# Kernel tuning notes

Measured on AMD Instinct MI355X. Metric: run time of the kernel, lower is better.

Reference implementation:

```python
import jax, jax.numpy as jnp
import numpy as np

EMB = 1024
HEADS = 16
EPS = 1e-6


def setup_inputs() -> dict:
    key = jax.random.key(0)
    ks = jax.random.split(key, 12)
    B, S, D = 2, 2048, EMB
    scale = 1.0 / np.sqrt(D)
    inp = {
        "v": jax.random.normal(ks[0], (B, S, D), jnp.float32),
        "k": jax.random.normal(ks[1], (B, S, D), jnp.float32),
        "q": jax.random.normal(ks[2], (B, S, D), jnp.float32),
        "Wv": jax.random.normal(ks[3], (D, D), jnp.float32) * scale,
        "bv": jnp.zeros((D,), jnp.float32),
        "Wk": jax.random.normal(ks[4], (D, D), jnp.float32) * scale,
        "bk": jnp.zeros((D,), jnp.float32),
        "Wq": jax.random.normal(ks[5], (D, D), jnp.float32) * scale,
        "bq": jnp.zeros((D,), jnp.float32),
        "Wo": jax.random.normal(ks[6], (D, D), jnp.float32) * scale,
        "bo": jnp.zeros((D,), jnp.float32),
        "gamma": jnp.ones((D,), jnp.float32),
        "beta": jnp.zeros((D,), jnp.float32),
    }
    return inp


def reference(v, k, q, Wv, bv, Wk, bk, Wq, bq, Wo, bo, gamma, beta):
    B, S, D = q.shape
    H = HEADS
    d = D // H  # head depth

    def split_heads(x):  # [B,S,D] -> [B,H,S,d]
        return x.reshape(B, S, H, d).transpose(0, 2, 1, 3)

    V = split_heads(v @ Wv + bv)
    K = split_heads(k @ Wk + bk)
    Q = split_heads(q @ Wq + bq)

    # scaled dot-product attention (full score matrix, no mask)
    scores = jnp.einsum("bhqd,bhkd->bhqk", Q, K) / jnp.sqrt(jnp.float32(d))
    attn = jax.nn.softmax(scores, axis=-1)
    ctx = jnp.einsum("bhqk,bhkd->bhqd", attn, V)

    ctx = ctx.transpose(0, 2, 1, 3).reshape(B, S, D)
    out = ctx @ Wo + bo + q  # final dense + residual

    # LayerNormalization(epsilon=1e-6) over last axis
    mu = jnp.mean(out, axis=-1, keepdims=True)
    var = jnp.var(out, axis=-1, keepdims=True)
    return gamma * (out - mu) * jax.lax.rsqrt(var + EPS) + beta
```

## Files before the change

kernel.cpp:

```cpp
#include <hip/hip_runtime.h>
#include <hip/hip_bf16.h>
#include <math.h>

#define D_EMB 1024
#define NBATCH 2
#define SEQ 2048
#define NH 16
#define HDIM 64
#define MTOT (NBATCH*SEQ)
#define NT (SEQ/64)

typedef unsigned short u16;
typedef __attribute__((ext_vector_type(8))) short bf16x8;
typedef __attribute__((ext_vector_type(4))) float f32x4;
typedef __attribute__((ext_vector_type(16))) float f32x16;
typedef __attribute__((ext_vector_type(4))) unsigned short u16x4;
typedef __attribute__((ext_vector_type(4))) unsigned int u32x4;

__device__ __forceinline__ u16 f2b(float f) {
  union { float f; unsigned u; } x; x.f = f;
  unsigned r = x.u + 0x7fffu + ((x.u >> 16) & 1u);
  return (u16)(r >> 16);
}

__device__ __forceinline__ void gld_lds16(const u16* g, u16* l) {
  __builtin_amdgcn_global_load_lds(
      (const __attribute__((address_space(1))) void*)g,
      (__attribute__((address_space(3))) void*)l, 16, 0, 0);
}

__global__ __launch_bounds__(256) void convert_qkv(
    const float* __restrict__ v, const float* __restrict__ k, const float* __restrict__ q,
    u16* __restrict__ vb, u16* __restrict__ kb, u16* __restrict__ qb) {
  int idx = blockIdx.x * 256 + threadIdx.x;
  float4 a;
  u16x4 o;
  a = ((const float4*)v)[idx];
  o.x = f2b(a.x); o.y = f2b(a.y); o.z = f2b(a.z); o.w = f2b(a.w);
  ((u16x4*)vb)[idx] = o;
  a = ((const float4*)k)[idx];
  o.x = f2b(a.x); o.y = f2b(a.y); o.z = f2b(a.z); o.w = f2b(a.w);
  ((u16x4*)kb)[idx] = o;
  a = ((const float4*)q)[idx];
  o.x = f2b(a.x); o.y = f2b(a.y); o.z = f2b(a.z); o.w = f2b(a.w);
  ((u16x4*)qb)[idx] = o;
}

__global__ __launch_bounds__(256) void transpose_w(
    const float* __restrict__ Wv, const float* __restrict__ Wk,
    const float* __restrict__ Wq, const float* __restrict__ Wo,
    u16* __restrict__ Wvt, u16* __restrict__ Wkt,
    u16* __restrict__ Wqt, u16* __restrict__ Wot) {
  __shared__ float tile[32][33];
  int z = blockIdx.z;
  const float* W = (z==0) ? Wv : (z==1) ? Wk : (z==2) ? Wq : Wo;
  u16* Wt = (z==0) ? Wvt : (z==1) ? Wkt : (z==2) ? Wqt : Wot;
  int tx = threadIdx.x, ty = threadIdx.y;
  int n0 = blockIdx.x * 32, k0 = blockIdx.y * 32;
#pragma unroll
  for (int i = 0; i < 4; ++i)
    tile[ty + i*8][tx] = W[(size_t)(k0 + ty + i*8) * D_EMB + n0 + tx];
  __syncthreads();
#pragma unroll
  for (int i = 0; i < 4; ++i)
    Wt[(size_t)(n0 + ty + i*8) * D_EMB + k0 + tx] = f2b(tile[tx][ty + i*8]);
}

__device__ __forceinline__ void gemm_loop(
    const u16* __restrict__ A, const u16* __restrict__ Bt,
    u16* lds_a, u16* lds_b, int bm, int bn, int wid, int lane,
    int wr, int wc, f32x4 acc[4][4]) {
#pragma unroll 1
  for (int kt = 0; kt < D_EMB/64; ++kt) {
    __syncthreads();
#pragma unroll
    for (int i = 0; i < 4; ++i) {
      int chunk = i*4 + wid;
      int row = chunk*8 + (lane >> 3);
      int slot = (lane & 7) ^ (row & 7);
      const u16* srcA = A + (size_t)(bm*128 + row) * D_EMB + kt*64 + slot*8;
      gld_lds16(srcA, lds_a + chunk*512);
      const u16* srcB = Bt + (size_t)(bn*128 + row) * D_EMB + kt*64 + slot*8;
      gld_lds16(srcB, lds_b + chunk*512);
    }
    __syncthreads();
#pragma unroll
    for (int st = 0; st < 2; ++st) {
      bf16x8 af[4], bfr[4];
#pragma unroll
      for (int mb = 0; mb < 4; ++mb) {
        int row = wr*64 + mb*16 + (lane & 15);
        int slot = (st*4 + (lane >> 4)) ^ (row & 7);
        af[mb] = *(const bf16x8*)(lds_a + row*64 + slot*8);
      }
#pragma unroll
      for (int nb = 0; nb < 4; ++nb) {
        int row = wc*64 + nb*16 + (lane & 15);
        int slot = (st*4 + (lane >> 4)) ^ (row & 7);
        bfr[nb] = *(const bf16x8*)(lds_b + row*64 + slot*8);
      }
#pragma unroll
      for (int mb = 0; mb < 4; ++mb)
#pragma unroll
        for (int nb = 0; nb < 4; ++nb)
          acc[mb][nb] = __builtin_amdgcn_mfma_f32_16x16x32_bf16(af[mb], bfr[nb], acc[mb][nb], 0, 0, 0);
    }
  }
}

__global__ __launch_bounds__(256) void gemm_qkv(
    const u16* __restrict__ vb, const u16* __restrict__ kb, const u16* __restrict__ qb,
    const u16* __restrict__ Wvt, const u16* __restrict__ Wkt, const u16* __restrict__ Wqt,
    const float* __restrict__ bv, const float* __restrict__ bk, const float* __restrict__ bq,
    u16* __restrict__ Vt, u16* __restrict__ Kh, u16* __restrict__ Qh) {
  __shared__ u16 lds_a[128*64];
  __shared__ u16 lds_b[128*64];
  int z = blockIdx.z;
  const u16* A  = (z==0) ? vb : (z==1) ? kb : qb;
  const u16* Bt = (z==0) ? Wvt : (z==1) ? Wkt : Wqt;
  const float* bias = (z==0) ? bv : (z==1) ? bk : bq;
  int tid = threadIdx.x, wid = tid >> 6, lane = tid & 63;
  int wr = wid >> 1, wc = wid & 1;
  int bm = blockIdx.y, bn = blockIdx.x;
  f32x4 acc[4][4];
#pragma unroll
  for (int i = 0; i < 4; ++i)
#pragma unroll
    for (int j = 0; j < 4; ++j) acc[i][j] = (f32x4){0.f,0.f,0.f,0.f};
  gemm_loop(A, Bt, lds_a, lds_b, bm, bn, wid, lane, wr, wc, acc);
  int g = lane >> 4, c = lane & 15;
#pragma unroll
  for (int mb = 0; mb < 4; ++mb) {
    int row0 = bm*128 + wr*64 + mb*16 + g*4;
#pragma unroll
    for (int nb = 0; nb < 4; ++nb) {
      int col = bn*128 + wc*64 + nb*16 + c;
      float bsv = bias[col];
      int h = col >> 6, dd = col & 63;
      if (z == 2) {
#pragma unroll
        for (int r = 0; r < 4; ++r) {
          int m = row0 + r; int b = m >> 11, s = m & (SEQ-1);
          float val = (acc[mb][nb][r] + bsv) * 0.18033688f;
          Qh[(((size_t)b*NH + h)*SEQ + s)*HDIM + dd] = f2b(val);
        }
      } else if (z == 1) {
#pragma unroll
        for (int r = 0; r < 4; ++r) {
          int m = row0 + r; int b = m >> 11, s = m & (SEQ-1);
          Kh[(((size_t)b*NH + h)*SEQ + s)*HDIM + dd] = f2b(acc[mb][nb][r] + bsv);
        }
      } else {
        int m = row0; int b = m >> 11, s = m & (SEQ-1);
        u16x4 pk;
        pk.x = f2b(acc[mb][nb][0] + bsv);
        pk.y = f2b(acc[mb][nb][1] + bsv);
        pk.z = f2b(acc[mb][nb][2] + bsv);
        pk.w = f2b(acc[mb][nb][3] + bsv);
        *(u16x4*)(Vt + (((size_t)b*NH + h)*HDIM + dd)*SEQ + s) = pk;
      }
    }
  }
}

__global__ __launch_bounds__(256, 2) void attn_k(
    const u16* __restrict__ Qh, const u16* __restrict__ Kh,
    const u16* __restrict__ Vt, u16* __restrict__ ctx) {
  __shared__ u16 kt_lds[2][64*64];
  __shared__ u16 vt_lds[2][64*64];
  const int tid = threadIdx.x, wid = tid >> 6, lane = tid & 63;
  const int lo5 = lane & 31, hi = lane >> 5;
  const int bh = blockIdx.y;
  const int qb = blockIdx.x * 128 + wid * 32;
  const size_t base = (size_t)bh * SEQ * HDIM;

  const int srow = tid >> 3;
  const int c0 = (tid & 7) ^ (srow & 7) ^ (srow >> 3);
  const int c1 = c0 ^ 4;
  const u16* kp0 = Kh + base + (size_t)srow * HDIM + c0*8;
  const u16* kp1 = Kh + base + (size_t)(srow+32) * HDIM + c1*8;
  const u16* vp0 = Vt + base + (size_t)srow * SEQ + c0*8;
  const u16* vp1 = Vt + base + (size_t)(srow+32) * SEQ + c1*8;

  const int r7 = lo5 & 7, r3 = lo5 >> 3;
  int offs0[4], offs1[4];
#pragma unroll
  for (int t = 0; t < 4; ++t) {
    int p = (2*t + hi) ^ r7 ^ r3;
    offs0[t] = lo5*128 + p*16;
    offs1[t] = (lo5+32)*128 + (p^4)*16;
  }
  const char* ktbase = (const char*)&kt_lds[0][0];
  const char* vtbase = (const char*)&vt_lds[0][0];

  bf16x8 qf[4];
#pragma unroll
  for (int t = 0; t < 4; ++t)
    qf[t] = *(const bf16x8*)(Qh + base + (size_t)(qb + lo5)*HDIM + t*16 + hi*8);

  bf16x8 onesf;
#pragma unroll
  for (int j = 0; j < 8; ++j) onesf[j] = (short)0x3F80;
  f32x16 z16;
#pragma unroll
  for (int i = 0; i < 16; ++i) z16[i] = 0.f;

  f32x16 o0, o1, lacc;
#pragma unroll
  for (int i = 0; i < 16; ++i) { o0[i] = 0.f; o1[i] = 0.f; lacc[i] = 0.f; }
  float m = -1e30f;
  const float THR = 11.5f;

#define STAGE(B) do { \
    gld_lds16(kp0, &kt_lds[B][wid*512]); \
    gld_lds16(kp1, &kt_lds[B][2048 + wid*512]); \
    gld_lds16(vp0, &vt_lds[B][wid*512]); \
    gld_lds16(vp1, &vt_lds[B][2048 + wid*512]); \
    kp0 += 64*HDIM; kp1 += 64*HDIM; vp0 += 64; vp1 += 64; \
  } while (0)

#define TILE(B, VMSTR, DOSTAGE) do { \
    asm volatile("s_waitcnt " VMSTR ::: "memory"); \
    __builtin_amdgcn_sched_barrier(0); \
    __builtin_amdgcn_s_barrier();             \
    __builtin_amdgcn_sched_barrier(0); \
    const char* kb_ = ktbase + (B)*8192; \
    const char* vb_ = vtbase + (B)*8192; \
    bf16x8 kf0[4], kf1[4], vf0[4], vf1[4]; \
    _Pragma("unroll") for (int t = 0; t < 4; ++t) { \
      kf0[t] = *(const bf16x8*)(kb_ + offs0[t]); \
      kf1[t] = *(const bf16x8*)(kb_ + offs1[t]); \
      vf0[t] = *(const bf16x8*)(vb_ + offs0[t]); \
      vf1[t] = *(const bf16x8*)(vb_ + offs1[t]); } \
    asm volatile("s_waitcnt lgkmcnt(0)" ::: "memory"); \
    __builtin_amdgcn_sched_barrier(0); \
    __builtin_amdgcn_s_barrier();             \
    __builtin_amdgcn_sched_barrier(0); \
    if (DOSTAGE) { STAGE(B); } \
    __builtin_amdgcn_sched_barrier(0); \
    __builtin_amdgcn_s_setprio(1); \
    f32x16 st0 = __builtin_amdgcn_mfma_f32_32x32x16_bf16(kf0[0], qf[0], z16, 0, 0, 0); \
    f32x16 st1 = __builtin_amdgcn_mfma_f32_32x32x16_bf16(kf1[0], qf[0], z16, 0, 0, 0); \
    _Pragma("unroll") for (int t = 1; t < 4; ++t) { \
      st0 = __builtin_amdgcn_mfma_f32_32x32x16_bf16(kf0[t], qf[t], st0, 0, 0, 0); \
      st1 = __builtin_amdgcn_mfma_f32_32x32x16_bf16(kf1[t], qf[t], st1, 0, 0, 0); } \
    __builtin_amdgcn_s_setprio(0); \
    float pm = fmaxf(fmaxf(st0[0], st0[1]), st0[2]); \
    _Pragma("unroll") for (int r = 3; r < 15; r += 3) \
      pm = fmaxf(fmaxf(fmaxf(pm, st0[r]), st0[r+1]), st0[r+2]); \
    pm = fmaxf(pm, st0[15]); \
    _Pragma("unroll") for (int r = 0; r < 15; r += 3) \
      pm = fmaxf(fmaxf(fmaxf(pm, st1[r]), st1[r+1]), st1[r+2]); \
    pm = fmaxf(pm, st1[15]); \
    pm = fmaxf(pm, __shfl_xor(pm, 32)); \
    if (__any(pm > m + THR)) { \
      float mn = fmaxf(m, pm); \
      float scl = exp2f(m - mn); \
      m = mn; \
      _Pragma("unroll") for (int r = 0; r < 16; ++r) { \
        int crow = (r & 3) + 8*(r >> 2) + 4*hi; \
        float sr = __int_as_float( \
            __builtin_amdgcn_ds_bpermute(crow << 2, __float_as_int(scl))); \
        o0[r] *= sr; o1[r] *= sr; lacc[r] *= sr; } } \
    _Pragma("unroll") for (int r = 0; r < 16; ++r) st0[r] = exp2f(st0[r] - m); \
    _Pragma("unroll") for (int r = 0; r < 16; ++r) st1[r] = exp2f(st1[r] - m); \
    bf16x8 pa[4]; \
    _Pragma("unroll") for (int ks = 0; ks < 2; ++ks) { \
      const f32x16& s_ = ks ? st1 : st0; \
      unsigned X[8]; \
      _Pragma("unroll") for (int w = 0; w < 8; ++w) { \
        float lo_f = s_[2*w], hi_f = s_[2*w + 1]; \
        asm("v_cvt_pk_bf16_f32 %0, %1, %2" : "=v"(X[w]) : "v"(lo_f), "v"(hi_f)); } \
      asm volatile("v_permlane32_swap_b32 %0, %1" : "+v"(X[0]), "+v"(X[2])); \
      asm volatile("v_permlane32_swap_b32 %0, %1" : "+v"(X[1]), "+v"(X[3])); \
      asm volatile("v_permlane32_swap_b32 %0, %1" : "+v"(X[4]), "+v"(X[6])); \
      asm volatile("v_permlane32_swap_b32 %0, %1" : "+v"(X[5]), "+v"(X[7])); \
      union { u32x4 u; bf16x8 b; } cva, cvb; \
      cva.u = (u32x4){X[0], X[1], X[2], X[3]}; \
      cvb.u = (u32x4){X[4], X[5], X[6], X[7]}; \
      pa[2*ks]   = cva.b; \
      pa[2*ks+1] = cvb.b; } \
    __builtin_amdgcn_s_setprio(1); \
    _Pragma("unroll") for (int t = 0; t < 4; ++t) { \
      o0 = __builtin_amdgcn_mfma_f32_32x32x16_bf16(pa[t], vf0[t], o0, 0, 0, 0); \
      o1 = __builtin_amdgcn_mfma_f32_32x32x16_bf16(pa[t], vf1[t], o1, 0, 0, 0); } \
    _Pragma("unroll") for (int t = 0; t < 4; ++t) \
      lacc = __builtin_amdgcn_mfma_f32_32x32x16_bf16(pa[t], onesf, lacc, 0, 0, 0); \
    __builtin_amdgcn_s_setprio(0); \
  } while (0)

  STAGE(0);
  STAGE(1);

#pragma unroll 1
  for (int kv = 0; kv < NT - 2; kv += 2) {
    TILE(0, "vmcnt(4)", 1);
    TILE(1, "vmcnt(4)", 1);
  }
  TILE(0, "vmcnt(4)", 0);
  TILE(1, "vmcnt(0)", 0);

#undef STAGE
#undef TILE

  const int b = bh >> 4, h = bh & 15;
#pragma unroll
  for (int r = 0; r < 16; ++r) {
    int crow = (r & 3) + 8*(r >> 2) + 4*hi;
    float lr = 1.0f / lacc[r];
    int s = qb + crow;
    u16* row = ctx + ((size_t)(b*SEQ + s))*D_EMB + h*64;
    row[lo5]      = f2b(o0[r] * lr);
    row[32 + lo5] = f2b(o1[r] * lr);
  }
}

__global__ __launch_bounds__(256) void gemm_out(
    const u16* __restrict__ ctx, const u16* __restrict__ Wot,
    const float* __restrict__ bo, const float* __restrict__ resid,
    float* __restrict__ preln) {
  __shared__ u16 lds_a[128*64];
  __shared__ u16 lds_b[128*64];
  int tid = threadIdx.x, wid = tid >> 6, lane = tid & 63;
  int wr = wid >> 1, wc = wid & 1;
  int bm = blockIdx.y, bn = blockIdx.x;
  f32x4 acc[4][4];
#pragma unroll
  for (int i = 0; i < 4; ++i)
#pragma unroll
    for (int j = 0; j < 4; ++j) acc[i][j] = (f32x4){0.f,0.f,0.f,0.f};
  gemm_loop(ctx, Wot, lds_a, lds_b, bm, bn, wid, lane, wr, wc, acc);
  int g = lane >> 4, c = lane & 15;
#pragma unroll
  for (int mb = 0; mb < 4; ++mb) {
    int row0 = bm*128 + wr*64 + mb*16 + g*4;
#pragma unroll
    for (int nb = 0; nb < 4; ++nb) {
      int col = bn*128 + wc*64 + nb*16 + c;
      float bsv = bo[col];
#pragma unroll
      for (int r = 0; r < 4; ++r) {
        int m = row0 + r;
        preln[(size_t)m*D_EMB + col] = acc[mb][nb][r] + bsv + resid[(size_t)m*D_EMB + col];
      }
    }
  }
}

__global__ __launch_bounds__(256) void ln_k(
    const float* __restrict__ preln, const float* __restrict__ gamma,
    const float* __restrict__ beta, float* __restrict__ out) {
  int row = blockIdx.x, tid = threadIdx.x;
  float4 x = ((const float4*)(preln + (size_t)row*D_EMB))[tid];
  float s  = x.x + x.y + x.z + x.w;
  float ss = x.x*x.x + x.y*x.y + x.z*x.z + x.w*x.w;
#pragma unroll
  for (int off = 32; off; off >>= 1) {
    s  += __shfl_xor(s, off);
    ss += __shfl_xor(ss, off);
  }
  __shared__ float red_s[4], red_ss[4];
  int wid = tid >> 6, lane = tid & 63;
  if (lane == 0) { red_s[wid] = s; red_ss[wid] = ss; }
  __syncthreads();
  s  = red_s[0] + red_s[1] + red_s[2] + red_s[3];
  ss = red_ss[0] + red_ss[1] + red_ss[2] + red_ss[3];
  float mu = s * (1.0f/1024.0f);
  float var = ss * (1.0f/1024.0f) - mu*mu;
  float rstd = rsqrtf(var + 1e-6f);
  float4 gm = ((const float4*)gamma)[tid];
  float4 bt = ((const float4*)beta)[tid];
  float4 y;
  y.x = (x.x - mu)*rstd*gm.x + bt.x;
  y.y = (x.y - mu)*rstd*gm.y + bt.y;
  y.z = (x.z - mu)*rstd*gm.z + bt.z;
  y.w = (x.w - mu)*rstd*gm.w + bt.w;
  ((float4*)(out + (size_t)row*D_EMB))[tid] = y;
}

extern "C" void kernel_launch(void* const* d_in, const int* in_sizes, int n_in,
                              void* d_out, int out_size, void* d_ws, size_t ws_size,
                              hipStream_t stream) {
  const float* v_in  = (const float*)d_in[0];
  const float* k_in  = (const float*)d_in[1];
  const float* q_in  = (const float*)d_in[2];
  const float* Wv    = (const float*)d_in[3];
  const float* bv    = (const float*)d_in[4];
  const float* Wk    = (const float*)d_in[5];
  const float* bk    = (const float*)d_in[6];
  const float* Wq    = (const float*)d_in[7];
  const float* bq    = (const float*)d_in[8];
  const float* Wo    = (const float*)d_in[9];
  const float* bo    = (const float*)d_in[10];
  const float* gamma = (const float*)d_in[11];
  const float* beta  = (const float*)d_in[12];
  char* ws = (char*)d_ws;

  const size_t TOKB = (size_t)MTOT * D_EMB * 2;
  const size_t WB   = (size_t)D_EMB * D_EMB * 2;
  size_t o_qb = 0;
  size_t o_kb = o_qb + TOKB;
  size_t o_vb = o_kb + TOKB;
  size_t o_wq = o_vb + TOKB;
  size_t o_wk = o_wq + WB;
  size_t o_wv = o_wk + WB;
  size_t o_wo = o_wv + WB;
  size_t o_Qh = o_wo + WB;
  size_t o_Kh = o_Qh + TOKB;
  size_t o_Vt = o_Kh + TOKB;
  size_t o_cx = o_Vt + TOKB;

  u16* qb  = (u16*)(ws + o_qb);
  u16* kb  = (u16*)(ws + o_kb);
  u16* vb  = (u16*)(ws + o_vb);
  u16* wqt = (u16*)(ws + o_wq);
  u16* wkt = (u16*)(ws + o_wk);
  u16* wvt = (u16*)(ws + o_wv);
  u16* wot = (u16*)(ws + o_wo);
  u16* Qh  = (u16*)(ws + o_Qh);
  u16* Kh  = (u16*)(ws + o_Kh);
  u16* Vt  = (u16*)(ws + o_Vt);
  u16* cx  = (u16*)(ws + o_cx);
  float* preln = (float*)(ws + 0);

  convert_qkv<<<4096, 256, 0, stream>>>(v_in, k_in, q_in, vb, kb, qb);
  transpose_w<<<dim3(32, 32, 4), dim3(32, 8), 0, stream>>>(Wv, Wk, Wq, Wo, wvt, wkt, wqt, wot);
  gemm_qkv<<<dim3(8, 32, 3), 256, 0, stream>>>(vb, kb, qb, wvt, wkt, wqt, bv, bk, bq, Vt, Kh, Qh);
  attn_k<<<dim3(16, 32), 256, 0, stream>>>(Qh, Kh, Vt, cx);
  gemm_out<<<dim3(8, 32), 256, 0, stream>>>(cx, wot, bo, q_in, preln);
  ln_k<<<4096, 256, 0, stream>>>(preln, gamma, beta, (float*)d_out);
}
```

Measured before the change: 159.2 us.

## Deepen attention K/V LDS pipeline to four buffers and prefetch next K fragments

Expands the attention kernel's LDS ring from two to four K/V tiles and restructures each tile step. QK^T and softmax now run on K fragments read during the previous step, while V reads for the current tile and K reads for the next tile are issued behind the global-load barrier. This overlaps LDS reads with MFMA and exp work and drops one barrier per tile. In exchange, LDS use doubles to 64KB per block, which may limit occupancy at two blocks per CU, and more fragments stay live in registers across tiles. The row-max reduction is also reordered into a pairwise interleave.

```diff
diff --git a/kernel.cpp b/kernel.cpp
--- a/kernel.cpp
+++ b/kernel.cpp
@@ -166,8 +166,8 @@
 __global__ __launch_bounds__(256, 2) void attn_k(
     const u16* __restrict__ Qh, const u16* __restrict__ Kh,
     const u16* __restrict__ Vt, u16* __restrict__ ctx) {
-  __shared__ u16 kt_lds[2][64*64];
-  __shared__ u16 vt_lds[2][64*64];
+  __shared__ u16 kt_lds[4][64*64];
+  __shared__ u16 vt_lds[4][64*64];
   const int tid = threadIdx.x, wid = tid >> 6, lane = tid & 63;
   const int lo5 = lane & 31, hi = lane >> 5;
   const int bh = blockIdx.y;
@@ -211,6 +211,9 @@
   float m = -1e30f;
   const float THR = 11.5f;
 
+  bf16x8 kf0[4], kf1[4];
+  bf16x8 vf0[4], vf1[4];
+
 #define STAGE(B) do { \
     gld_lds16(kp0, &kt_lds[B][wid*512]); \
     gld_lds16(kp1, &kt_lds[B][2048 + wid*512]); \
@@ -219,25 +222,21 @@
     kp0 += 64*HDIM; kp1 += 64*HDIM; vp0 += 64; vp1 += 64; \
   } while (0)
 
-#define TILE(B, VMSTR, DOSTAGE) do { \
-    asm volatile("s_waitcnt " VMSTR ::: "memory"); \
-    __builtin_amdgcn_sched_barrier(0); \
-    __builtin_amdgcn_s_barrier();             \
-    __builtin_amdgcn_sched_barrier(0); \
+#define READK(B) do { \
     const char* kb_ = ktbase + (B)*8192; \
-    const char* vb_ = vtbase + (B)*8192; \
-    bf16x8 kf0[4], kf1[4], vf0[4], vf1[4]; \
     _Pragma("unroll") for (int t = 0; t < 4; ++t) { \
       kf0[t] = *(const bf16x8*)(kb_ + offs0[t]); \
-      kf1[t] = *(const bf16x8*)(kb_ + offs1[t]); \
+      kf1[t] = *(const bf16x8*)(kb_ + offs1[t]); } \
+  } while (0)
+
+#define READV(B) do { \
+    const char* vb_ = vtbase + (B)*8192; \
+    _Pragma("unroll") for (int t = 0; t < 4; ++t) { \
       vf0[t] = *(const bf16x8*)(vb_ + offs0[t]); \
       vf1[t] = *(const bf16x8*)(vb_ + offs1[t]); } \
-    asm volatile("s_waitcnt lgkmcnt(0)" ::: "memory"); \
-    __builtin_amdgcn_sched_barrier(0); \
-    __builtin_amdgcn_s_barrier();             \
-    __builtin_amdgcn_sched_barrier(0); \
-    if (DOSTAGE) { STAGE(B); } \
-    __builtin_amdgcn_sched_barrier(0); \
+  } while (0)
+
+#define QKT_SM() \
     __builtin_amdgcn_s_setprio(1); \
     f32x16 st0 = __builtin_amdgcn_mfma_f32_32x32x16_bf16(kf0[0], qf[0], z16, 0, 0, 0); \
     f32x16 st1 = __builtin_amdgcn_mfma_f32_32x32x16_bf16(kf1[0], qf[0], z16, 0, 0, 0); \
@@ -245,13 +244,9 @@
       st0 = __builtin_amdgcn_mfma_f32_32x32x16_bf16(kf0[t], qf[t], st0, 0, 0, 0); \
       st1 = __builtin_amdgcn_mfma_f32_32x32x16_bf16(kf1[t], qf[t], st1, 0, 0, 0); } \
     __builtin_amdgcn_s_setprio(0); \
-    float pm = fmaxf(fmaxf(st0[0], st0[1]), st0[2]); \
-    _Pragma("unroll") for (int r = 3; r < 15; r += 3) \
-      pm = fmaxf(fmaxf(fmaxf(pm, st0[r]), st0[r+1]), st0[r+2]); \
-    pm = fmaxf(pm, st0[15]); \
-    _Pragma("unroll") for (int r = 0; r < 15; r += 3) \
-      pm = fmaxf(fmaxf(fmaxf(pm, st1[r]), st1[r+1]), st1[r+2]); \
-    pm = fmaxf(pm, st1[15]); \
+    float pm = fmaxf(st0[0], st1[0]); \
+    _Pragma("unroll") for (int r = 1; r < 16; ++r) \
+      pm = fmaxf(pm, fmaxf(st0[r], st1[r])); \
     pm = fmaxf(pm, __shfl_xor(pm, 32)); \
     if (__any(pm > m + THR)) { \
       float mn = fmaxf(m, pm); \
@@ -263,7 +258,9 @@
             __builtin_amdgcn_ds_bpermute(crow << 2, __float_as_int(scl))); \
         o0[r] *= sr; o1[r] *= sr; lacc[r] *= sr; } } \
     _Pragma("unroll") for (int r = 0; r < 16; ++r) st0[r] = exp2f(st0[r] - m); \
-    _Pragma("unroll") for (int r = 0; r < 16; ++r) st1[r] = exp2f(st1[r] - m); \
+    _Pragma("unroll") for (int r = 0; r < 16; ++r) st1[r] = exp2f(st1[r] - m);
+
+#define CVT_PA() \
     bf16x8 pa[4]; \
     _Pragma("unroll") for (int ks = 0; ks < 2; ++ks) { \
       const f32x16& s_ = ks ? st1 : st0; \
@@ -279,28 +276,68 @@
       cva.u = (u32x4){X[0], X[1], X[2], X[3]}; \
       cvb.u = (u32x4){X[4], X[5], X[6], X[7]}; \
       pa[2*ks]   = cva.b; \
-      pa[2*ks+1] = cvb.b; } \
+      pa[2*ks+1] = cvb.b; }
+
+#define PV() \
     __builtin_amdgcn_s_setprio(1); \
     _Pragma("unroll") for (int t = 0; t < 4; ++t) { \
       o0 = __builtin_amdgcn_mfma_f32_32x32x16_bf16(pa[t], vf0[t], o0, 0, 0, 0); \
       o1 = __builtin_amdgcn_mfma_f32_32x32x16_bf16(pa[t], vf1[t], o1, 0, 0, 0); } \
     _Pragma("unroll") for (int t = 0; t < 4; ++t) \
       lacc = __builtin_amdgcn_mfma_f32_32x32x16_bf16(pa[t], onesf, lacc, 0, 0, 0); \
-    __builtin_amdgcn_s_setprio(0); \
+    __builtin_amdgcn_s_setprio(0);
+
+#define TILE(B, VMSTR, DOSTAGE, SB) do { \
+    asm volatile("s_waitcnt lgkmcnt(0)" ::: "memory");    \
+    __builtin_amdgcn_sched_barrier(0); \
+    QKT_SM() \
+    asm volatile("s_waitcnt " VMSTR ::: "memory");        \
+    __builtin_amdgcn_sched_barrier(0); \
+    __builtin_amdgcn_s_barrier(); \
+    __builtin_amdgcn_sched_barrier(0); \
+    if (DOSTAGE) { STAGE(SB); } \
+    READV(B);                  \
+    READK((B+1)&3);            \
+    CVT_PA()                   \
+    asm volatile("s_waitcnt lgkmcnt(8)" ::: "memory");    \
+    __builtin_amdgcn_sched_barrier(0); \
+    PV() \
   } while (0)
 
-  STAGE(0);
-  STAGE(1);
+  STAGE(0); STAGE(1); STAGE(2);
+  asm volatile("s_waitcnt vmcnt(8)" ::: "memory");
+  __builtin_amdgcn_sched_barrier(0);
+  __builtin_amdgcn_s_barrier();
+  __builtin_amdgcn_sched_barrier(0);
+  READK(0);
 
 #pragma unroll 1
-  for (int kv = 0; kv < NT - 2; kv += 2) {
-    TILE(0, "vmcnt(4)", 1);
-    TILE(1, "vmcnt(4)", 1);
-  }
-  TILE(0, "vmcnt(4)", 0);
-  TILE(1, "vmcnt(0)", 0);
+  for (int kv = 0; kv < NT - 4; kv += 4) {
+    TILE(0, "vmcnt(4)", 1, 3);
+    TILE(1, "vmcnt(4)", 1, 0);
+    TILE(2, "vmcnt(4)", 1, 1);
+    TILE(3, "vmcnt(4)", 1, 2);
+  }
+  TILE(0, "vmcnt(4)", 1, 3);
+  TILE(1, "vmcnt(4)", 0, 0);
+  TILE(2, "vmcnt(0)", 0, 0);
+  {
+    asm volatile("s_waitcnt lgkmcnt(0)" ::: "memory");
+    __builtin_amdgcn_sched_barrier(0);
+    QKT_SM()
+    READV(3);
+    CVT_PA()
+    asm volatile("s_waitcnt lgkmcnt(0)" ::: "memory");
+    __builtin_amdgcn_sched_barrier(0);
+    PV()
+  }
 
 #undef STAGE
+#undef READK
+#undef READV
+#undef QKT_SM
+#undef CVT_PA
+#undef PV
 #undef TILE
 
   const int b = bh >> 4, h = bh & 15;
```

Result: slower. 165.6 us (+4.0%).
